# Kernel tuning notes

Measured on AMD Instinct MI355X. Metric: run time of the kernel, lower is better.

Reference implementation:

```python
import jax, jax.numpy as jnp
import numpy as np

NUM_BASIS = 10
CUTOFF = 1.0
SQRT3 = 3.0 ** 0.5
SMOOTH_C = 1.14136 * float(np.exp(2.0))  # e3nn smooth_finite constant


def soft_unit_step(x):
    # e3nn soft_unit_step: exp(-1/x) for x>0 else 0 (nan-safe for grads)
    xs = jnp.where(x > 0, x, 1.0)
    return jnp.where(x > 0, jnp.exp(-1.0 / xs), 0.0)


def smooth_finite_embed(length):
    # soft_one_hot_linspace(start=0, end=cutoff, number=NUM_BASIS,
    #                       basis='smooth_finite', cutoff=True), then * sqrt(NUM_BASIS)
    values = jnp.linspace(0.0, CUTOFF, NUM_BASIS + 2)
    step = values[1] - values[0]
    values = values[1:-1]                      # [NUM_BASIS]
    diff = (length[:, None] - values) / step   # [E, NUM_BASIS]
    f = SMOOTH_C * soft_unit_step(diff + 1.0) * soft_unit_step(1.0 - diff)
    return f * (NUM_BASIS ** 0.5)


def sh_lmax2_norm(vec):
    # e3nn o3.spherical_harmonics(lmax=2, normalize=True, normalization='norm')
    r = jnp.linalg.norm(vec, axis=-1, keepdims=True)
    u = vec / jnp.where(r > 0, r, 1.0)
    x, y, z = u[:, 0], u[:, 1], u[:, 2]
    sh0 = jnp.ones_like(x)                       # l=0
    sh2_0 = SQRT3 * x * z                        # l=2 block ('norm' normalized)
    sh2_1 = SQRT3 * x * y
    sh2_2 = y * y - 0.5 * (x * x + z * z)
    sh2_3 = SQRT3 * y * z
    sh2_4 = (SQRT3 / 2.0) * (z * z - x * x)
    return jnp.stack([sh0, x, y, z, sh2_0, sh2_1, sh2_2, sh2_3, sh2_4], axis=-1)


def setup_inputs() -> dict:
    key = jax.random.key(0)
    k1, k2, k3, k4 = jax.random.split(key, 4)
    pos = jax.random.uniform(k1, (100000, 3), dtype=jnp.float32)
    query_pos = jax.random.uniform(k2, (8, 1250, 3), dtype=jnp.float32)
    # Surrogate for torch_cluster.radius(x, y, r=1.2*cutoff): fixed-size edge list
    edge_src = jax.random.randint(k3, (4000000,), 0, 10000)   # indexes flattened queries
    edge_dst = jax.random.randint(k4, (4000000,), 0, 100000)  # indexes points
    return {"pos": pos, "query_pos": query_pos, "edge_src": edge_src, "edge_dst": edge_dst}


def reference(pos, query_pos, edge_src, edge_dst):
    y = query_pos.reshape(-1, 3)                 # [Nt*Ny, 3]
    edge_vec = y[edge_src] - pos[edge_dst]       # [E, 3] irregular gather
    edge_length = jnp.linalg.norm(edge_vec, axis=-1)
    edge_length_embedded = smooth_finite_embed(edge_length)  # [E, 10]
    edge_sh = sh_lmax2_norm(edge_vec)                         # [E, 9]
    return edge_sh, edge_length_embedded
```

## Files before the change

kernel.cpp:

```cpp
#include <hip/hip_runtime.h>


#define SQRT3F 1.7320508075688772f
#define EMB_K 26.6692997f
#define TPB 256
#define EPB 256
#define NQF 30000
#define NSH4 (EPB * 9 / 4)
#define NEM4 (EPB * 10 / 4)
#define QSH_GRID 1024

typedef float floatx4 __attribute__((ext_vector_type(4)));

__global__ __launch_bounds__(256) void pad_kernel(
    const float* __restrict__ pos, float4* __restrict__ pos4, int npos)
{
    int i = blockIdx.x * blockDim.x + threadIdx.x;
    if (i < npos)
        pos4[i] = make_float4(pos[3 * i + 0], pos[3 * i + 1], pos[3 * i + 2], 0.f);
}

__device__ __forceinline__ void compute_edge(
    float ax, float ay, float az, float bx, float by, float bz,
    float* __restrict__ sh, float2* __restrict__ em2)
{
    float vx = ax - bx, vy = ay - by, vz = az - bz;
    float r2 = vx * vx + vy * vy + vz * vz;
    float r = sqrtf(r2);
    float inv = (r > 0.f) ? (1.f / r) : 1.f;
    float x = vx * inv, y = vy * inv, z = vz * inv;

    sh[0] = 1.f;
    sh[1] = x;
    sh[2] = y;
    sh[3] = z;
    sh[4] = SQRT3F * x * z;
    sh[5] = SQRT3F * x * y;
    sh[6] = y * y - 0.5f * (x * x + z * z);
    sh[7] = SQRT3F * y * z;
    sh[8] = 0.5f * SQRT3F * (z * z - x * x);

#pragma unroll
    for (int j = 0; j < 5; ++j) em2[j] = make_float2(0.f, 0.f);

    float t = r * 11.f;
    int k = (int)t;
    float* e = (float*)em2;
#pragma unroll
    for (int m = 0; m < 2; ++m) {
        int j = k - 1 + m;
        float a = t - (float)j;
        float b = (float)(j + 2) - t;
        if (j >= 0 && j < 10 && a > 0.f && b > 0.f)
            e[j] = EMB_K * __expf(-(__frcp_rn(a) + __frcp_rn(b)));
    }
}

template <bool PAD>
__global__ __launch_bounds__(256, 1) void qsh_kernel(
    const float* __restrict__ pos,
    const float* __restrict__ qpos,
    const float4* __restrict__ pos4,
    const int* __restrict__ esrc,
    const int* __restrict__ edst,
    float* __restrict__ out_sh,
    float* __restrict__ out_emb,
    int n)
{
    __shared__ float qp[NQF];
    __shared__ __align__(16) float sh_lds[EPB * 9];
    __shared__ __align__(16) float emb_lds[EPB * 10];

    const int tid = threadIdx.x;

    {
        const floatx4* src = (const floatx4*)qpos;
        floatx4* dst = (floatx4*)qp;
        for (int i = tid; i < NQF / 4; i += TPB) dst[i] = src[i];
    }
    __syncthreads();

    const int nchunk = (n + EPB - 1) / EPB;
    const int G = gridDim.x;
    int c = blockIdx.x;
    if (c >= nchunk) return;

    int e0 = c * EPB + tid; if (e0 >= n) e0 = n - 1;
    int s0 = __builtin_nontemporal_load(esrc + e0);
    int d0 = __builtin_nontemporal_load(edst + e0);
    float bx0, by0, bz0;
    if (PAD) { float4 t = pos4[d0]; bx0 = t.x; by0 = t.y; bz0 = t.z; }
    else { bx0 = pos[3*d0]; by0 = pos[3*d0+1]; bz0 = pos[3*d0+2]; }

    int c1 = c + G;
    int s1 = s0, d1 = d0;
    if (c1 < nchunk) {
        int e1 = c1 * EPB + tid; if (e1 >= n) e1 = n - 1;
        s1 = __builtin_nontemporal_load(esrc + e1);
        d1 = __builtin_nontemporal_load(edst + e1);
    }

    while (true) {
        float ax = qp[3 * s0], ay = qp[3 * s0 + 1], az = qp[3 * s0 + 2];
        compute_edge(ax, ay, az, bx0, by0, bz0,
                     sh_lds + tid * 9, (float2*)(emb_lds + tid * 10));

        const bool have1 = (c1 < nchunk);
        float bx1 = bx0, by1 = by0, bz1 = bz0;
        if (have1) {
            if (PAD) { float4 t = pos4[d1]; bx1 = t.x; by1 = t.y; bz1 = t.z; }
            else { bx1 = pos[3*d1]; by1 = pos[3*d1+1]; bz1 = pos[3*d1+2]; }
        }
        int c2 = c1 + G, s2 = s1, d2 = d1;
        if (have1 && c2 < nchunk) {
            int e2 = c2 * EPB + tid; if (e2 >= n) e2 = n - 1;
            s2 = __builtin_nontemporal_load(esrc + e2);
            d2 = __builtin_nontemporal_load(edst + e2);
        }

        asm volatile("s_waitcnt lgkmcnt(0)" ::: "memory");
        __builtin_amdgcn_s_barrier();
        __builtin_amdgcn_sched_barrier(0);

        const int base = c * EPB;
        const int count = min(EPB, n - base);
        floatx4* osh4 = (floatx4*)(out_sh + (size_t)base * 9);
        floatx4* oem4 = (floatx4*)(out_emb + (size_t)base * 10);
        const floatx4* shv = (const floatx4*)sh_lds;
        const floatx4* emv = (const floatx4*)emb_lds;
        if (count == EPB) {
#pragma unroll
            for (int k = 0; k < 3; ++k) {
                int i4 = k * TPB + tid;
                if (i4 < NSH4)
                    __builtin_nontemporal_store(shv[i4], osh4 + i4);
            }
#pragma unroll
            for (int k = 0; k < 3; ++k) {
                int i4 = k * TPB + tid;
                if (i4 < NEM4)
                    __builtin_nontemporal_store(emv[i4], oem4 + i4);
            }
        } else {
            float* osh = out_sh + (size_t)base * 9;
            float* oem = out_emb + (size_t)base * 10;
            int nsh = count * 9;
            for (int idx = tid; idx < nsh; idx += TPB)
                __builtin_nontemporal_store(sh_lds[idx], osh + idx);
            int nem = count * 10;
            for (int idx = tid; idx < nem; idx += TPB)
                __builtin_nontemporal_store(emb_lds[idx], oem + idx);
        }

        asm volatile("s_waitcnt lgkmcnt(0)" ::: "memory");
        __builtin_amdgcn_s_barrier();
        __builtin_amdgcn_sched_barrier(0);

        if (!have1) break;
        c = c1; c1 = c2;
        s0 = s1; d0 = d1; bx0 = bx1; by0 = by1; bz0 = bz1;
        s1 = s2; d1 = d2;
    }
}

extern "C" void kernel_launch(void* const* d_in, const int* in_sizes, int n_in,
                              void* d_out, int out_size, void* d_ws, size_t ws_size,
                              hipStream_t stream) {
    const float* pos  = (const float*)d_in[0];
    const float* qpos = (const float*)d_in[1];
    const int* esrc = (const int*)d_in[2];
    const int* edst = (const int*)d_in[3];
    int npos = in_sizes[0] / 3;
    int nq   = in_sizes[1] / 3;
    (void)nq;
    int n    = in_sizes[2];

    float* out_sh  = (float*)d_out;
    float* out_emb = out_sh + (size_t)n * 9;

    size_t need = (size_t)npos * sizeof(float4);
    if (ws_size >= need) {
        float4* pos4 = (float4*)d_ws;
        int pgrid = (npos + TPB - 1) / TPB;
        pad_kernel<<<pgrid, TPB, 0, stream>>>(pos, pos4, npos);
        qsh_kernel<true><<<QSH_GRID, TPB, 0, stream>>>(
            pos, qpos, pos4, esrc, edst, out_sh, out_emb, n);
    } else {
        qsh_kernel<false><<<QSH_GRID, TPB, 0, stream>>>(
            pos, qpos, nullptr, esrc, edst, out_sh, out_emb, n);
    }
}
```

Measured before the change: 400.0 us.

## Use 1024-thread blocks with two-phase half-chunk LDS staging

Block size and edges per chunk go from 256 to 1024, and the grid shrinks from 1024 to 256 blocks, so the 120 KB query-position copy into LDS is made by a quarter as many blocks. To fit LDS, the staging buffers hold only 512 edges: each chunk is computed and written back in two halves, with extra barriers between the phases. This cuts redundant query-table loading, but it adds barriers and leaves half of each block idle during each compute phase.

```diff
diff --git a/kernel.cpp b/kernel.cpp
--- a/kernel.cpp
+++ b/kernel.cpp
@@ -3,12 +3,11 @@
 
 #define SQRT3F 1.7320508075688772f
 #define EMB_K 26.6692997f
-#define TPB 256
-#define EPB 256
+#define TPB 1024
+#define EPB 1024
+#define HALF 512
 #define NQF 30000
-#define NSH4 (EPB * 9 / 4)
-#define NEM4 (EPB * 10 / 4)
-#define QSH_GRID 1024
+#define QSH_GRID 256
 
 typedef float floatx4 __attribute__((ext_vector_type(4)));
 
@@ -56,11 +55,45 @@
     }
 }
 
+__device__ __forceinline__ void writeback_half(
+    const float* __restrict__ sh_lds, const float* __restrict__ emb_lds,
+    float* __restrict__ out_sh, float* __restrict__ out_emb,
+    size_t obase, int h, int tid)
+{
+    if (h == HALF) {
+        floatx4* osh4 = (floatx4*)(out_sh + obase * 9);
+        floatx4* oem4 = (floatx4*)(out_emb + obase * 10);
+        const floatx4* shv = (const floatx4*)sh_lds;
+        const floatx4* emv = (const floatx4*)emb_lds;
+        __builtin_nontemporal_store(shv[tid], osh4 + tid);
+        if (tid + TPB < 1152)
+            __builtin_nontemporal_store(shv[tid + TPB], osh4 + tid + TPB);
+        __builtin_nontemporal_store(emv[tid], oem4 + tid);
+        if (tid + TPB < 1280)
+            __builtin_nontemporal_store(emv[tid + TPB], oem4 + tid + TPB);
+    } else {
+        float* osh = out_sh + obase * 9;
+        float* oem = out_emb + obase * 10;
+        int nsh = h * 9;
+        for (int idx = tid; idx < nsh; idx += TPB)
+            __builtin_nontemporal_store(sh_lds[idx], osh + idx);
+        int nem = h * 10;
+        for (int idx = tid; idx < nem; idx += TPB)
+            __builtin_nontemporal_store(emb_lds[idx], oem + idx);
+    }
+}
+
+#define LDS_BARRIER() do {                                   \
+    asm volatile("s_waitcnt lgkmcnt(0)" ::: "memory");       \
+    __builtin_amdgcn_s_barrier();                            \
+    __builtin_amdgcn_sched_barrier(0);                       \
+} while (0)
+
 template <bool PAD>
-__global__ __launch_bounds__(256, 1) void qsh_kernel(
+__global__ __launch_bounds__(1024, 1) void qsh_kernel(
     const float* __restrict__ pos,
     const float* __restrict__ qpos,
-    const float4* __restrict__ pos4,
+    const floatx4* __restrict__ pos4,
     const int* __restrict__ esrc,
     const int* __restrict__ edst,
     float* __restrict__ out_sh,
@@ -68,8 +101,8 @@
     int n)
 {
     __shared__ float qp[NQF];
-    __shared__ __align__(16) float sh_lds[EPB * 9];
-    __shared__ __align__(16) float emb_lds[EPB * 10];
+    __shared__ __align__(16) float sh_lds[HALF * 9];
+    __shared__ __align__(16) float emb_lds[HALF * 10];
 
     const int tid = threadIdx.x;
 
@@ -89,7 +122,7 @@
     int s0 = __builtin_nontemporal_load(esrc + e0);
     int d0 = __builtin_nontemporal_load(edst + e0);
     float bx0, by0, bz0;
-    if (PAD) { float4 t = pos4[d0]; bx0 = t.x; by0 = t.y; bz0 = t.z; }
+    if (PAD) { floatx4 t = pos4[d0]; bx0 = t.x; by0 = t.y; bz0 = t.z; }
     else { bx0 = pos[3*d0]; by0 = pos[3*d0+1]; bz0 = pos[3*d0+2]; }
 
     int c1 = c + G;
@@ -101,14 +134,19 @@
     }
 
     while (true) {
+        const int base = c * EPB;
+        const int count = min(EPB, n - base);
+
         float ax = qp[3 * s0], ay = qp[3 * s0 + 1], az = qp[3 * s0 + 2];
-        compute_edge(ax, ay, az, bx0, by0, bz0,
-                     sh_lds + tid * 9, (float2*)(emb_lds + tid * 10));
+
+        if (tid < HALF && tid < count)
+            compute_edge(ax, ay, az, bx0, by0, bz0,
+                         sh_lds + tid * 9, (float2*)(emb_lds + tid * 10));
 
         const bool have1 = (c1 < nchunk);
         float bx1 = bx0, by1 = by0, bz1 = bz0;
         if (have1) {
-            if (PAD) { float4 t = pos4[d1]; bx1 = t.x; by1 = t.y; bz1 = t.z; }
+            if (PAD) { floatx4 t = pos4[d1]; bx1 = t.x; by1 = t.y; bz1 = t.z; }
             else { bx1 = pos[3*d1]; by1 = pos[3*d1+1]; bz1 = pos[3*d1+2]; }
         }
         int c2 = c1 + G, s2 = s1, d2 = d1;
@@ -118,43 +156,26 @@
             d2 = __builtin_nontemporal_load(edst + e2);
         }
 
-        asm volatile("s_waitcnt lgkmcnt(0)" ::: "memory");
-        __builtin_amdgcn_s_barrier();
-        __builtin_amdgcn_sched_barrier(0);
-
-        const int base = c * EPB;
-        const int count = min(EPB, n - base);
-        floatx4* osh4 = (floatx4*)(out_sh + (size_t)base * 9);
-        floatx4* oem4 = (floatx4*)(out_emb + (size_t)base * 10);
-        const floatx4* shv = (const floatx4*)sh_lds;
-        const floatx4* emv = (const floatx4*)emb_lds;
-        if (count == EPB) {
-#pragma unroll
-            for (int k = 0; k < 3; ++k) {
-                int i4 = k * TPB + tid;
-                if (i4 < NSH4)
-                    __builtin_nontemporal_store(shv[i4], osh4 + i4);
-            }
-#pragma unroll
-            for (int k = 0; k < 3; ++k) {
-                int i4 = k * TPB + tid;
-                if (i4 < NEM4)
-                    __builtin_nontemporal_store(emv[i4], oem4 + i4);
-            }
-        } else {
-            float* osh = out_sh + (size_t)base * 9;
-            float* oem = out_emb + (size_t)base * 10;
-            int nsh = count * 9;
-            for (int idx = tid; idx < nsh; idx += TPB)
-                __builtin_nontemporal_store(sh_lds[idx], osh + idx);
-            int nem = count * 10;
-            for (int idx = tid; idx < nem; idx += TPB)
-                __builtin_nontemporal_store(emb_lds[idx], oem + idx);
-        }
-
-        asm volatile("s_waitcnt lgkmcnt(0)" ::: "memory");
-        __builtin_amdgcn_s_barrier();
-        __builtin_amdgcn_sched_barrier(0);
+        LDS_BARRIER();
+
+        int h1 = min(HALF, count);
+        writeback_half(sh_lds, emb_lds, out_sh, out_emb, (size_t)base, h1, tid);
+
+        LDS_BARRIER();
+
+        if (tid >= HALF && tid < count)
+            compute_edge(ax, ay, az, bx0, by0, bz0,
+                         sh_lds + (tid - HALF) * 9,
+                         (float2*)(emb_lds + (tid - HALF) * 10));
+
+        LDS_BARRIER();
+
+        int h2 = count - HALF;
+        if (h2 > 0)
+            writeback_half(sh_lds, emb_lds, out_sh, out_emb,
+                           (size_t)(base + HALF), h2, tid);
+
+        LDS_BARRIER();
 
         if (!have1) break;
         c = c1; c1 = c2;
@@ -171,8 +192,6 @@
     const int* esrc = (const int*)d_in[2];
     const int* edst = (const int*)d_in[3];
     int npos = in_sizes[0] / 3;
-    int nq   = in_sizes[1] / 3;
-    (void)nq;
     int n    = in_sizes[2];
 
     float* out_sh  = (float*)d_out;
@@ -181,10 +200,10 @@
     size_t need = (size_t)npos * sizeof(float4);
     if (ws_size >= need) {
         float4* pos4 = (float4*)d_ws;
-        int pgrid = (npos + TPB - 1) / TPB;
-        pad_kernel<<<pgrid, TPB, 0, stream>>>(pos, pos4, npos);
+        int pgrid = (npos + 255) / 256;
+        pad_kernel<<<pgrid, 256, 0, stream>>>(pos, pos4, npos);
         qsh_kernel<true><<<QSH_GRID, TPB, 0, stream>>>(
-            pos, qpos, pos4, esrc, edst, out_sh, out_emb, n);
+            pos, qpos, (const floatx4*)pos4, esrc, edst, out_sh, out_emb, n);
     } else {
         qsh_kernel<false><<<QSH_GRID, TPB, 0, stream>>>(
             pos, qpos, nullptr, esrc, edst, out_sh, out_emb, n);
```

Result: faster. 350.7 us (-12.3%).
